# Performance work log

Hardware: AMD Instinct MI355X
Metric: run time of the kernel (lower is better)

The kernel has to match this reference:

```python
import jax, jax.numpy as jnp
import numpy as np

NUM_TOPICS = 100
VOCAB = 8192
MC_N = 20
MD_N = 20
LAMBDA_D = 0.7
LAMBDA_A = 100.0
WARMUP_RATIO = 0.5
NUM_EPOCHS = 200


def setup_inputs() -> dict:
    key = jax.random.key(0)
    k1, k2 = jax.random.split(key)
    beta = jax.random.normal(k1, (NUM_TOPICS, VOCAB), dtype=jnp.float32)
    W = jax.random.uniform(k2, (VOCAB, VOCAB), dtype=jnp.float32)
    # fill_diagonal_(1) in __init__
    d = jnp.arange(VOCAB)
    W = W.at[d, d].set(1.0)
    return {"beta": beta, "coherence_weight": W, "epoch": 120}


def reference(beta, coherence_weight, epoch):
    K, V = beta.shape
    rows = jnp.arange(K)[:, None]

    # --- Mc: top-Mc_n mask -> additive -99999 on non-topk entries ---
    _, mc_idx = jax.lax.top_k(beta, MC_N)                      # [K, Mc_n]
    Mc = jnp.zeros_like(beta).at[rows, mc_idx].set(1.0)        # [K, V]
    Mc_add = (1.0 - Mc) * (-99999.0)

    # softmax over masked beta is detached in the original
    p = jax.lax.stop_gradient(jax.nn.softmax(beta + Mc_add, axis=1))
    M = p @ coherence_weight                                    # [K, V]

    # row-wise min-max normalize, then Wc = 1 - normalized
    m_min = jnp.min(M, axis=1, keepdims=True)
    m_max = jnp.max(M, axis=1, keepdims=True)
    Wc = 1.0 - (M - m_min) / (m_max - m_min)

    loss = 100.0 * jax.nn.softmax(beta, axis=1) ** 2 * Wc       # [K, V]

    # --- diversity mask Md (lambda_d > 0.5 branch) ---
    _, md_idx = jax.lax.top_k(beta, MD_N)
    Md_mask = jnp.zeros_like(beta).at[rows, md_idx].set(1.0)    # [K, V]
    # Md[t, v] = any other row has v in its top-Md_n
    col_sum = jnp.sum(Md_mask, axis=0)                          # [V]
    Md = (col_sum[None, :] - Md_mask) > 0                       # [K, V] bool

    pos = jnp.sum(jnp.where(Md, loss, 0.0))
    neg = jnp.sum(jnp.where(Md, 0.0, loss))
    total = (pos * LAMBDA_D + neg * (1.0 - LAMBDA_D)) * 2.0

    warmup_epochs = int(WARMUP_RATIO * NUM_EPOCHS)              # 100
    lambda_a_delta = LAMBDA_A / warmup_epochs
    lambda_a = epoch * lambda_a_delta if epoch < warmup_epochs else LAMBDA_A
    return lambda_a * total
```

## Files before the change

kernel.cpp:

```cpp
#include <hip/hip_runtime.h>
#include <math.h>

#define NT 100
#define VOCAB 8192
#define TOPN 20
#define NSL 8
#define SCOLS 1024
#define SCAP 128
#define CHUNKS 8
#define CCOLS 1024
#define NB (NT * CHUNKS)

__global__ __launch_bounds__(256) void slice_kernel(
    const float* __restrict__ beta,
    float* __restrict__ cand_val,
    int*   __restrict__ cand_idx,
    int*   __restrict__ sl_cnt,
    float* __restrict__ sl_max,
    float* __restrict__ sl_sum)
{
    const int b = blockIdx.x;
    const int t = threadIdx.x;
    const int k = b / NSL;
    const int s = b % NSL;
    const int col0 = s * SCOLS;

    __shared__ float sred[4];
    __shared__ int   sredi[4];
    __shared__ int   s_cnt;

    const float4 v = *reinterpret_cast<const float4*>(
        beta + (size_t)k * VOCAB + col0 + t * 4);

    float mx = fmaxf(fmaxf(v.x, v.y), fmaxf(v.z, v.w));
#pragma unroll
    for (int off = 32; off >= 1; off >>= 1) mx = fmaxf(mx, __shfl_down(mx, off));
    if ((t & 63) == 0) sred[t >> 6] = mx;
    __syncthreads();
    const float smax = fmaxf(fmaxf(sred[0], sred[1]), fmaxf(sred[2], sred[3]));
    __syncthreads();

    float se = expf(v.x - smax) + expf(v.y - smax) + expf(v.z - smax) + expf(v.w - smax);
#pragma unroll
    for (int off = 32; off >= 1; off >>= 1) se += __shfl_down(se, off);
    if ((t & 63) == 0) sred[t >> 6] = se;
    __syncthreads();
    const float ssum = sred[0] + sred[1] + sred[2] + sred[3];
    __syncthreads();

    float T = smax - 1.5f;
    for (int g = 0; g < 8; ++g) {
        int c = ((v.x >= T) ? 1 : 0) + ((v.y >= T) ? 1 : 0)
              + ((v.z >= T) ? 1 : 0) + ((v.w >= T) ? 1 : 0);
#pragma unroll
        for (int off = 32; off >= 1; off >>= 1) c += __shfl_down(c, off);
        if ((t & 63) == 0) sredi[t >> 6] = c;
        __syncthreads();
        const int cnt = sredi[0] + sredi[1] + sredi[2] + sredi[3];
        if (cnt >= TOPN) break;
        T -= 0.4f;
        __syncthreads();
    }
    if (t == 0) s_cnt = 0;
    __syncthreads();

#pragma unroll
    for (int e = 0; e < 4; ++e) {
        const float val = (&v.x)[e];
        const bool  pr  = (val >= T);
        const unsigned long long mask = __ballot(pr);
        const int lane = t & 63;
        const int pre  = __popcll(mask & ((1ull << lane) - 1ull));
        int base = 0;
        if (lane == 0) base = atomicAdd(&s_cnt, __popcll(mask));
        base = __shfl(base, 0);
        if (pr) {
            const int p = base + pre;
            if (p < SCAP) {
                cand_val[(size_t)b * SCAP + p] = val;
                cand_idx[(size_t)b * SCAP + p] = col0 + t * 4 + e;
            }
        }
    }
    __syncthreads();
    if (t == 0) {
        sl_cnt[b] = min(s_cnt, SCAP);
        sl_max[b] = smax;
        sl_sum[b] = ssum;
    }
}

__global__ __launch_bounds__(256) void merge_kernel(
    const float* __restrict__ cand_val,
    const int*   __restrict__ cand_idx,
    const int*   __restrict__ sl_cnt,
    const float* __restrict__ sl_max,
    const float* __restrict__ sl_sum,
    int*   __restrict__ top_idx,
    float* __restrict__ top_p,
    float* __restrict__ rowstats)
{
    const int k = blockIdx.x;
    const int t = threadIdx.x;

    __shared__ int   scnt[NSL];
    __shared__ int   soff[NSL + 1];
    __shared__ float smaxs[NSL], ssums[NSL];
    __shared__ float cval[NSL * SCAP];
    __shared__ int   cidx[NSL * SCAP];
    __shared__ float s_winv[TOPN];
    __shared__ int   s_wini[TOPN];
    __shared__ float s_ps, s_rowmax;

    if (t < NSL) {
        scnt[t]  = sl_cnt[k * NSL + t];
        smaxs[t] = sl_max[k * NSL + t];
        ssums[t] = sl_sum[k * NSL + t];
    }
    __syncthreads();
    if (t == 0) {
        int o = 0;
#pragma unroll
        for (int s = 0; s < NSL; ++s) { soff[s] = o; o += scnt[s]; }
        soff[NSL] = o;
        float rm = smaxs[0];
#pragma unroll
        for (int s = 1; s < NSL; ++s) rm = fmaxf(rm, smaxs[s]);
        s_rowmax = rm;
    }
    __syncthreads();
    const int total = soff[NSL];
    const float rowmax = s_rowmax;

#pragma unroll
    for (int s = 0; s < NSL; ++s) {
        const int n = scnt[s], o = soff[s];
        for (int p = t; p < n; p += 256) {
            cval[o + p] = cand_val[(size_t)(k * NSL + s) * SCAP + p];
            cidx[o + p] = cand_idx[(size_t)(k * NSL + s) * SCAP + p];
        }
    }
    __syncthreads();

    if (t < 64) {
        for (int it = 0; it < TOPN; ++it) {
            float bv = -INFINITY; int bp = -1;
            for (int p = t; p < total; p += 64) {
                const float vv = cval[p];
                if (vv > bv) { bv = vv; bp = p; }
            }
#pragma unroll
            for (int off = 32; off >= 1; off >>= 1) {
                const float ov = __shfl_down(bv, off);
                const int   op = __shfl_down(bp, off);
                if (ov > bv) { bv = ov; bp = op; }
            }
            bp = __shfl(bp, 0);
            bv = __shfl(bv, 0);
            if (t == 0) { s_winv[it] = bv; s_wini[it] = cidx[bp]; }
            cval[bp] = -INFINITY;
        }
    }
    __syncthreads();

    if (t == 0) {
        float ps = 0.f;
#pragma unroll
        for (int j = 0; j < TOPN; ++j) ps += expf(s_winv[j] - rowmax);
        s_ps = ps;
        float rs = 0.f;
#pragma unroll
        for (int s = 0; s < NSL; ++s) rs += ssums[s] * expf(smaxs[s] - rowmax);
        rowstats[2 * k + 0] = rowmax;
        rowstats[2 * k + 1] = rs;
    }
    __syncthreads();
    if (t < TOPN) {
        top_idx[k * TOPN + t] = s_wini[t];
        top_p[k * TOPN + t]   = expf(s_winv[t] - rowmax) / s_ps;
    }
}

__global__ __launch_bounds__(256) void fused_kernel(
    const float* __restrict__ beta,
    const float* __restrict__ W,
    const int*   __restrict__ top_idx,
    const float* __restrict__ top_p,
    const float* __restrict__ rowstats,
    float* __restrict__ part6)
{
    const int b = blockIdx.x;
    const int k = b / CHUNKS;
    const int c = b % CHUNKS;
    const int t = threadIdx.x;

    __shared__ int   sIdx[TOPN];
    __shared__ float sP[TOPN];
    __shared__ int   cnt[CCOLS];
    __shared__ float sA[4], sB[4], sC[4], sD[4], sE[4], sF[4];

    if (t < TOPN) { sIdx[t] = top_idx[k * TOPN + t]; sP[t] = top_p[k * TOPN + t]; }
#pragma unroll
    for (int i = 0; i < CCOLS / 256; ++i) cnt[i * 256 + t] = 0;
    __syncthreads();

    int   idx_r[TOPN];
    float p_r[TOPN];
#pragma unroll
    for (int j = 0; j < TOPN; ++j) { idx_r[j] = sIdx[j]; p_r[j] = sP[j]; }

    const int lo  = c * CCOLS;
    const int col = lo + t * 4;
    float4 w_r[TOPN];
#pragma unroll
    for (int j = 0; j < TOPN; ++j)
        w_r[j] = *reinterpret_cast<const float4*>(W + (size_t)idx_r[j] * VOCAB + col);
    const float4 bv = *reinterpret_cast<const float4*>(beta + (size_t)k * VOCAB + col);

#pragma unroll 8
    for (int e = t; e < NT * TOPN; e += 256) {
        const int v = top_idx[e] - lo;
        if ((unsigned)v < (unsigned)CCOLS) atomicAdd(&cnt[v], 1);
    }
    __syncthreads();
    if (t < TOPN) {
        const int v = sIdx[t] - lo;
        if ((unsigned)v < (unsigned)CCOLS) atomicSub(&cnt[v], 1);
    }

    float4 m = make_float4(0.f, 0.f, 0.f, 0.f);
#pragma unroll
    for (int j = 0; j < TOPN; ++j) {
        const float pj = p_r[j];
        m.x += pj * w_r[j].x; m.y += pj * w_r[j].y;
        m.z += pj * w_r[j].z; m.w += pj * w_r[j].w;
    }

    float mn  = fminf(fminf(m.x, m.y), fminf(m.z, m.w));
    float mxv = fmaxf(fmaxf(m.x, m.y), fmaxf(m.z, m.w));

    const float rmax = rowstats[2 * k + 0];
    const float rinv = 1.0f / rowstats[2 * k + 1];
    float4 w4;
    w4.x = expf(bv.x - rmax) * rinv;  w4.x = 100.f * w4.x * w4.x;
    w4.y = expf(bv.y - rmax) * rinv;  w4.y = 100.f * w4.y * w4.y;
    w4.z = expf(bv.z - rmax) * rinv;  w4.z = 100.f * w4.z * w4.z;
    w4.w = expf(bv.w - rmax) * rinv;  w4.w = 100.f * w4.w * w4.w;

    __syncthreads();

    float Apos = 0.f, Bpos = 0.f, Aneg = 0.f, Bneg = 0.f;
    {
        const int lc = t * 4;
        if (cnt[lc + 0] > 0) { Apos += w4.x; Bpos += w4.x * m.x; } else { Aneg += w4.x; Bneg += w4.x * m.x; }
        if (cnt[lc + 1] > 0) { Apos += w4.y; Bpos += w4.y * m.y; } else { Aneg += w4.y; Bneg += w4.y * m.y; }
        if (cnt[lc + 2] > 0) { Apos += w4.z; Bpos += w4.z * m.z; } else { Aneg += w4.z; Bneg += w4.z * m.z; }
        if (cnt[lc + 3] > 0) { Apos += w4.w; Bpos += w4.w * m.w; } else { Aneg += w4.w; Bneg += w4.w * m.w; }
    }

#pragma unroll
    for (int off = 32; off >= 1; off >>= 1) {
        mn   = fminf(mn,  __shfl_down(mn,  off));
        mxv  = fmaxf(mxv, __shfl_down(mxv, off));
        Apos += __shfl_down(Apos, off);
        Bpos += __shfl_down(Bpos, off);
        Aneg += __shfl_down(Aneg, off);
        Bneg += __shfl_down(Bneg, off);
    }
    if ((t & 63) == 0) {
        const int w = t >> 6;
        sA[w] = mn; sB[w] = mxv; sC[w] = Apos; sD[w] = Bpos; sE[w] = Aneg; sF[w] = Bneg;
    }
    __syncthreads();
    if (t == 0) {
        part6[b * 6 + 0] = fminf(fminf(sA[0], sA[1]), fminf(sA[2], sA[3]));
        part6[b * 6 + 1] = fmaxf(fmaxf(sB[0], sB[1]), fmaxf(sB[2], sB[3]));
        part6[b * 6 + 2] = sC[0] + sC[1] + sC[2] + sC[3];
        part6[b * 6 + 3] = sD[0] + sD[1] + sD[2] + sD[3];
        part6[b * 6 + 4] = sE[0] + sE[1] + sE[2] + sE[3];
        part6[b * 6 + 5] = sF[0] + sF[1] + sF[2] + sF[3];
    }
}

__global__ __launch_bounds__(128) void finalize_kernel(
    const float* __restrict__ part6,
    const int*   __restrict__ epoch,
    float* __restrict__ out)
{
    const int t = threadIdx.x;
    __shared__ float sp[128], sn[128];
    float pos = 0.f, neg = 0.f;
    if (t < NT) {
        float mn = INFINITY, mxv = -INFINITY;
        float Ap = 0.f, Bp = 0.f, An = 0.f, Bn = 0.f;
        for (int cc = 0; cc < CHUNKS; ++cc) {
            const float* p6 = part6 + (size_t)(t * CHUNKS + cc) * 6;
            mn  = fminf(mn,  p6[0]);
            mxv = fmaxf(mxv, p6[1]);
            Ap += p6[2]; Bp += p6[3]; An += p6[4]; Bn += p6[5];
        }
        const float inv = 1.0f / (mxv - mn);
        pos = Ap - inv * (Bp - mn * Ap);
        neg = An - inv * (Bn - mn * An);
    }
    sp[t] = pos; sn[t] = neg;
    __syncthreads();
    if (t == 0) {
        float P = 0.f, N = 0.f;
        for (int i = 0; i < NT; ++i) { P += sp[i]; N += sn[i]; }
        const float total = (P * 0.7f + N * 0.3f) * 2.0f;
        const int e = *epoch;
        const float la = (e < 100) ? (float)e : 100.0f;
        *out = la * total;
    }
}

extern "C" void kernel_launch(void* const* d_in, const int* in_sizes, int n_in,
                              void* d_out, int out_size, void* d_ws, size_t ws_size,
                              hipStream_t stream)
{
    (void)in_sizes; (void)n_in; (void)out_size; (void)ws_size;
    const float* beta  = (const float*)d_in[0];
    const float* W     = (const float*)d_in[1];
    const int*   epoch = (const int*)d_in[2];
    float* out = (float*)d_out;

    char* ws = (char*)d_ws;
    float* cand_val = (float*)ws;  ws += (size_t)NT * NSL * SCAP * sizeof(float);
    int*   cand_idx = (int*)ws;    ws += (size_t)NT * NSL * SCAP * sizeof(int);
    int*   sl_cnt   = (int*)ws;    ws += NT * NSL * sizeof(int);
    float* sl_max   = (float*)ws;  ws += NT * NSL * sizeof(float);
    float* sl_sum   = (float*)ws;  ws += NT * NSL * sizeof(float);
    int*   top_idx  = (int*)ws;    ws += NT * TOPN * sizeof(int);
    float* top_p    = (float*)ws;  ws += NT * TOPN * sizeof(float);
    float* rowstats = (float*)ws;  ws += NT * 2 * sizeof(float);
    float* part6    = (float*)ws;  ws += NB * 6 * sizeof(float);

    slice_kernel<<<NT * NSL, 256, 0, stream>>>(beta, cand_val, cand_idx,
                                               sl_cnt, sl_max, sl_sum);
    merge_kernel<<<NT, 256, 0, stream>>>(cand_val, cand_idx, sl_cnt, sl_max, sl_sum,
                                         top_idx, top_p, rowstats);
    fused_kernel<<<NB, 256, 0, stream>>>(beta, W, top_idx, top_p, rowstats, part6);
    finalize_kernel<<<1, 128, 0, stream>>>(part6, epoch, out);
}
```

Measured before the change: 49.18 us.

## Widen top-k slices and merge per-wave partial top-20 lists in parallel

The slice kernel now covers 2048 columns per block, with two float4 loads per thread, so there are 4 slices per row instead of 8 and each holds up to 256 candidates. The merge kernel gives each wave one slice and has it pick its own top-20 in parallel. A single wave then merges the 80 partial winners instead of one wave scanning every candidate 20 times. The row max is now taken from the top winner, and fewer, larger slice blocks may lower parallelism in the first kernel.

```diff
diff --git a/kernel.cpp b/kernel.cpp
--- a/kernel.cpp
+++ b/kernel.cpp
@@ -4,9 +4,9 @@
 #define NT 100
 #define VOCAB 8192
 #define TOPN 20
-#define NSL 8
-#define SCOLS 1024
-#define SCAP 128
+#define NSL 4
+#define SCOLS 2048
+#define SCAP 256
 #define CHUNKS 8
 #define CCOLS 1024
 #define NB (NT * CHUNKS)
@@ -29,10 +29,12 @@
     __shared__ int   sredi[4];
     __shared__ int   s_cnt;
 
-    const float4 v = *reinterpret_cast<const float4*>(
-        beta + (size_t)k * VOCAB + col0 + t * 4);
-
-    float mx = fmaxf(fmaxf(v.x, v.y), fmaxf(v.z, v.w));
+    const float* base = beta + (size_t)k * VOCAB + col0;
+    const float4 v0 = *reinterpret_cast<const float4*>(base + t * 4);
+    const float4 v1 = *reinterpret_cast<const float4*>(base + 1024 + t * 4);
+
+    float mx = fmaxf(fmaxf(fmaxf(v0.x, v0.y), fmaxf(v0.z, v0.w)),
+                     fmaxf(fmaxf(v1.x, v1.y), fmaxf(v1.z, v1.w)));
 #pragma unroll
     for (int off = 32; off >= 1; off >>= 1) mx = fmaxf(mx, __shfl_down(mx, off));
     if ((t & 63) == 0) sred[t >> 6] = mx;
@@ -40,7 +42,8 @@
     const float smax = fmaxf(fmaxf(sred[0], sred[1]), fmaxf(sred[2], sred[3]));
     __syncthreads();
 
-    float se = expf(v.x - smax) + expf(v.y - smax) + expf(v.z - smax) + expf(v.w - smax);
+    float se = expf(v0.x - smax) + expf(v0.y - smax) + expf(v0.z - smax) + expf(v0.w - smax)
+             + expf(v1.x - smax) + expf(v1.y - smax) + expf(v1.z - smax) + expf(v1.w - smax);
 #pragma unroll
     for (int off = 32; off >= 1; off >>= 1) se += __shfl_down(se, off);
     if ((t & 63) == 0) sred[t >> 6] = se;
@@ -49,9 +52,11 @@
     __syncthreads();
 
     float T = smax - 1.5f;
-    for (int g = 0; g < 8; ++g) {
-        int c = ((v.x >= T) ? 1 : 0) + ((v.y >= T) ? 1 : 0)
-              + ((v.z >= T) ? 1 : 0) + ((v.w >= T) ? 1 : 0);
+    for (int g = 0; g < 16; ++g) {
+        int c = ((v0.x >= T) ? 1 : 0) + ((v0.y >= T) ? 1 : 0)
+              + ((v0.z >= T) ? 1 : 0) + ((v0.w >= T) ? 1 : 0)
+              + ((v1.x >= T) ? 1 : 0) + ((v1.y >= T) ? 1 : 0)
+              + ((v1.z >= T) ? 1 : 0) + ((v1.w >= T) ? 1 : 0);
 #pragma unroll
         for (int off = 32; off >= 1; off >>= 1) c += __shfl_down(c, off);
         if ((t & 63) == 0) sredi[t >> 6] = c;
@@ -65,20 +70,24 @@
     __syncthreads();
 
 #pragma unroll
-    for (int e = 0; e < 4; ++e) {
-        const float val = (&v.x)[e];
-        const bool  pr  = (val >= T);
-        const unsigned long long mask = __ballot(pr);
-        const int lane = t & 63;
-        const int pre  = __popcll(mask & ((1ull << lane) - 1ull));
-        int base = 0;
-        if (lane == 0) base = atomicAdd(&s_cnt, __popcll(mask));
-        base = __shfl(base, 0);
-        if (pr) {
-            const int p = base + pre;
-            if (p < SCAP) {
-                cand_val[(size_t)b * SCAP + p] = val;
-                cand_idx[(size_t)b * SCAP + p] = col0 + t * 4 + e;
+    for (int i = 0; i < 2; ++i) {
+        const float4 rr = (i == 0) ? v0 : v1;
+#pragma unroll
+        for (int e = 0; e < 4; ++e) {
+            const float val = (&rr.x)[e];
+            const bool  pr  = (val >= T);
+            const unsigned long long mask = __ballot(pr);
+            const int lane = t & 63;
+            const int pre  = __popcll(mask & ((1ull << lane) - 1ull));
+            int bs = 0;
+            if (lane == 0) bs = atomicAdd(&s_cnt, __popcll(mask));
+            bs = __shfl(bs, 0);
+            if (pr) {
+                const int p = bs + pre;
+                if (p < SCAP) {
+                    cand_val[(size_t)b * SCAP + p] = val;
+                    cand_idx[(size_t)b * SCAP + p] = col0 + i * 1024 + t * 4 + e;
+                }
             }
         }
     }
@@ -102,15 +111,18 @@
 {
     const int k = blockIdx.x;
     const int t = threadIdx.x;
-
+    const int wv = t >> 6;
+    const int lane = t & 63;
+
+    __shared__ float cu[NSL * SCAP];
+    __shared__ int   cid[NSL * SCAP];
     __shared__ int   scnt[NSL];
-    __shared__ int   soff[NSL + 1];
     __shared__ float smaxs[NSL], ssums[NSL];
-    __shared__ float cval[NSL * SCAP];
-    __shared__ int   cidx[NSL * SCAP];
+    __shared__ float pv[NSL * TOPN];
+    __shared__ int   pid[NSL * TOPN];
     __shared__ float s_winv[TOPN];
     __shared__ int   s_wini[TOPN];
-    __shared__ float s_ps, s_rowmax;
+    __shared__ float s_ps;
 
     if (t < NSL) {
         scnt[t]  = sl_cnt[k * NSL + t];
@@ -118,36 +130,19 @@
         ssums[t] = sl_sum[k * NSL + t];
     }
     __syncthreads();
-    if (t == 0) {
-        int o = 0;
-#pragma unroll
-        for (int s = 0; s < NSL; ++s) { soff[s] = o; o += scnt[s]; }
-        soff[NSL] = o;
-        float rm = smaxs[0];
-#pragma unroll
-        for (int s = 1; s < NSL; ++s) rm = fmaxf(rm, smaxs[s]);
-        s_rowmax = rm;
-    }
-    __syncthreads();
-    const int total = soff[NSL];
-    const float rowmax = s_rowmax;
-
-#pragma unroll
-    for (int s = 0; s < NSL; ++s) {
-        const int n = scnt[s], o = soff[s];
-        for (int p = t; p < n; p += 256) {
-            cval[o + p] = cand_val[(size_t)(k * NSL + s) * SCAP + p];
-            cidx[o + p] = cand_idx[(size_t)(k * NSL + s) * SCAP + p];
-        }
-    }
-    __syncthreads();
-
-    if (t < 64) {
+
+    {
+        const int n = scnt[wv];
+        const size_t gbase = (size_t)(k * NSL + wv) * SCAP;
+        for (int p = lane; p < n; p += 64) {
+            cu[wv * SCAP + p]  = cand_val[gbase + p];
+            cid[wv * SCAP + p] = cand_idx[gbase + p];
+        }
         for (int it = 0; it < TOPN; ++it) {
             float bv = -INFINITY; int bp = -1;
-            for (int p = t; p < total; p += 64) {
-                const float vv = cval[p];
-                if (vv > bv) { bv = vv; bp = p; }
+            for (int p = lane; p < n; p += 64) {
+                const float v = cu[wv * SCAP + p];
+                if (v > bv) { bv = v; bp = p; }
             }
 #pragma unroll
             for (int off = 32; off >= 1; off >>= 1) {
@@ -157,13 +152,38 @@
             }
             bp = __shfl(bp, 0);
             bv = __shfl(bv, 0);
-            if (t == 0) { s_winv[it] = bv; s_wini[it] = cidx[bp]; }
-            cval[bp] = -INFINITY;
+            if (lane == 0) {
+                pv[wv * TOPN + it]  = bv;
+                pid[wv * TOPN + it] = (bp >= 0) ? cid[wv * SCAP + bp] : 0;
+            }
+            if (bp >= 0) cu[wv * SCAP + bp] = -INFINITY;
+        }
+    }
+    __syncthreads();
+
+    if (wv == 0) {
+        for (int it = 0; it < TOPN; ++it) {
+            float bv = -INFINITY; int bp = -1;
+            for (int p = lane; p < NSL * TOPN; p += 64) {
+                const float v = pv[p];
+                if (v > bv) { bv = v; bp = p; }
+            }
+#pragma unroll
+            for (int off = 32; off >= 1; off >>= 1) {
+                const float ov = __shfl_down(bv, off);
+                const int   op = __shfl_down(bp, off);
+                if (ov > bv) { bv = ov; bp = op; }
+            }
+            bp = __shfl(bp, 0);
+            bv = __shfl(bv, 0);
+            if (lane == 0) { s_winv[it] = bv; s_wini[it] = pid[bp]; }
+            pv[bp] = -INFINITY;
         }
     }
     __syncthreads();
 
     if (t == 0) {
+        const float rowmax = s_winv[0];
         float ps = 0.f;
 #pragma unroll
         for (int j = 0; j < TOPN; ++j) ps += expf(s_winv[j] - rowmax);
@@ -177,7 +197,7 @@
     __syncthreads();
     if (t < TOPN) {
         top_idx[k * TOPN + t] = s_wini[t];
-        top_p[k * TOPN + t]   = expf(s_winv[t] - rowmax) / s_ps;
+        top_p[k * TOPN + t]   = expf(s_winv[t] - s_winv[0]) / s_ps;
     }
 }
 
```

After: 49.95 us. No clear change (+1.6%).
